# Kernel tuning notes

Hardware: AMD Instinct MI355X
Metric: run time of the kernel (lower is better)

## Reference

```python
import jax, jax.numpy as jnp
import numpy as np

ALPHA = 0.7
BETA = 0.3
GAMMA = 4.0
SMALL_LESION_WEIGHT = 10.0
SMOOTH = 1e-05
AREA_THRESH = 100  # region.area < 100 -> small lesion


def _label_components(mask):
    """8-connectivity connected-component labeling via min-label flooding.
    mask: [B,H,W] bool. Returns int32 labels in [0, H*W) for foreground,
    H*W (sentinel) for background. Equivalent partitioning to skimage.measure.label."""
    B, H, W = mask.shape
    BIG = H * W
    ids = jnp.arange(BIG, dtype=jnp.int32).reshape(1, H, W)
    lab0 = jnp.where(mask, ids, BIG)

    def neighbor_min(lab):
        p = jnp.pad(lab, ((0, 0), (1, 1), (1, 1)), constant_values=BIG)
        m = lab
        for di in range(3):  # 3x3 window = self + 8-neighbors
            for dj in range(3):
                m = jnp.minimum(m, p[:, di:di + H, dj:dj + W])
        return jnp.where(mask, m, BIG)

    def cond(state):
        return state[1]

    def body(state):
        lab, _ = state
        new = neighbor_min(lab)
        return new, jnp.any(new != lab)

    lab, _ = jax.lax.while_loop(cond, body, (lab0, jnp.array(True)))
    return lab


def _small_lesion_weights(targets):
    """targets: [B,1,H,W] float. Returns [B,1,H,W] weights: small_lesion_weight on
    pixels of connected components with area < AREA_THRESH, else 1.0."""
    t = targets[:, 0]                      # [B,H,W]
    mask = t > 0.5
    B, H, W = mask.shape
    BIG = H * W
    lab = _label_components(mask)          # [B,H,W] int32
    flat_lab = lab.reshape(B, BIG)
    ones = mask.astype(jnp.float32).reshape(B, BIG)
    # per-image component areas; background pixels fall into segment BIG
    areas = jax.vmap(lambda l, o: jax.ops.segment_sum(o, l, num_segments=BIG + 1))(flat_lab, ones)
    pix_area = jnp.take_along_axis(areas, flat_lab, axis=1).reshape(B, H, W)
    small = mask & (pix_area < AREA_THRESH)
    w = jnp.where(small, SMALL_LESION_WEIGHT, 1.0)
    return w[:, None, :, :]


def _bce_with_logits(x, t):
    # numerically stable elementwise BCE-with-logits
    return jnp.maximum(x, 0.0) - x * t + jnp.log1p(jnp.exp(-jnp.abs(x)))


def setup_inputs() -> dict:
    key = jax.random.key(0)
    k1, k2 = jax.random.split(key)
    B, C, H, W = 8, 1, 1024, 1024
    predictions = jax.random.normal(k1, (B, C, H, W), dtype=jnp.float32)
    targets = (jax.random.uniform(k2, (B, C, H, W)) < 0.05).astype(jnp.float32)
    return {"predictions": predictions, "targets": targets}


def reference(predictions, targets):
    p = jax.nn.sigmoid(predictions)

    # dice loss (global)
    inter = jnp.sum(p * targets)
    union = jnp.sum(p) + jnp.sum(targets)
    dice_loss = 1.0 - (2.0 * inter + SMOOTH) / (union + SMOOTH)

    # focal loss from logits
    bce = _bce_with_logits(predictions, targets)
    is_pos = targets == 1
    p_t = jnp.where(is_pos, p, 1.0 - p)
    alpha_t = jnp.where(is_pos, ALPHA, 1.0 - ALPHA)
    focal_loss = jnp.mean(alpha_t * (1.0 - p_t) ** GAMMA * bce)

    # tversky loss (FN-focused)
    TP = inter
    FP = jnp.sum((1.0 - targets) * p)
    FN = jnp.sum(targets * (1.0 - p))
    tversky_loss = 1.0 - (TP + SMOOTH) / (TP + ALPHA * FP + BETA * FN + SMOOTH)

    # small-lesion weighted BCE (weights are a non-diff function of targets)
    w = _small_lesion_weights(jax.lax.stop_gradient(targets))
    small_lesion_loss = jnp.mean(w * bce)

    return (dice_loss + focal_loss + tversky_loss + small_lesion_loss) / 4.0
```

## Files before the change

kernel.cpp:

```cpp
#include <hip/hip_runtime.h>

typedef unsigned int u32;
typedef unsigned long long u64;

static constexpr int Bb = 8, Hh = 1024, Ww = 1024;
static constexpr int HW     = Hh * Ww;
static constexpr int NPIX   = Bb * HW;
static constexpr int NWORDS = NPIX / 64;
static constexpr int WPR    = Ww / 64;
static constexpr int WPI    = HW / 64;
static constexpr int NBK = 2048, NT = 256;
static constexpr int FNT = 512, FBG = 512;
static constexpr int SWORDS = NWORDS / FBG;
static constexpr int SPX    = SWORDS * 64;
static constexpr int CAP    = 2048;

static constexpr u32 POISON  = 0xAAAAAAAAu;
static constexpr u32 FLAGVAL = 0xC0FFEE00u;
static constexpr u32 LBITS  = 0x3FFFu;
static constexpr u32 BIGF   = 1u << 29;
static constexpr u32 CROSSF = 1u << 30;

__device__ inline u32 lab_load(u32* L, u32 i) {
    return __hip_atomic_load(&L[i], __ATOMIC_RELAXED, __HIP_MEMORY_SCOPE_AGENT);
}
__device__ inline void lab_store(u32* L, u32 i, u32 v) {
    __hip_atomic_store(&L[i], v, __ATOMIC_RELAXED, __HIP_MEMORY_SCOPE_AGENT);
}
__device__ inline u32 find_root(u32* L, u32 x) {
    while (true) {
        u32 p = lab_load(L, x);
        if (p >= (u32)NPIX || p == x) return x;
        x = p;
    }
}
__device__ inline void union_labels(u32* L, u32 a, u32 b) {
    while (true) {
        a = find_root(L, a);
        b = find_root(L, b);
        if (a == b) return;
        if (a < b) { u32 t = a; a = b; b = t; }
        u32 old = atomicMin(&L[a], b);
        if (old == a || old >= (u32)NPIX) return;
        a = old;
    }
}

__device__ inline u32 lds_load(u32* L, u32 x) {
    return __hip_atomic_load(&L[x], __ATOMIC_RELAXED, __HIP_MEMORY_SCOPE_WORKGROUP);
}
__device__ inline void lds_store(u32* L, u32 x, u32 v) {
    __hip_atomic_store(&L[x], v, __ATOMIC_RELAXED, __HIP_MEMORY_SCOPE_WORKGROUP);
}
__device__ inline u32 lfind2(u32* L, u32 x) {
    while (true) { u32 p = lds_load(L, x) & LBITS; if (p == x) return x; x = p; }
}
__device__ inline void lunion(u32* L, u32 a, u32 b) {
    while (true) {
        a = lfind2(L, a);
        b = lfind2(L, b);
        if (a == b) return;
        if (a < b) { u32 t = a; a = b; b = t; }
        u32 old = atomicMin(&L[a], b);
        if (old == a) return;
        a = old;
    }
}

__device__ inline double block_reduce(double v, double* lds) {
    for (int o = 32; o > 0; o >>= 1) v += __shfl_down(v, o, 64);
    int wave = threadIdx.x >> 6, lane = threadIdx.x & 63;
    __syncthreads();
    if (lane == 0) lds[wave] = v;
    __syncthreads();
    double r = 0.0;
    if (threadIdx.x == 0)
        for (int w = 0; w < (int)(blockDim.x >> 6); ++w) r += lds[w];
    return r;
}

__device__ inline float bce_pos(float x) {
    return fmaxf(-x, 0.0f) + __logf(1.0f + __expf(-fabsf(x)));
}

__device__ inline u64 spread4(u64 x) {
    x &= 0xFFFFull;
    x = (x | (x << 24)) & 0x000000FF000000FFull;
    x = (x | (x << 12)) & 0x000F000F000F000Full;
    x = (x | (x << 6))  & 0x0303030303030303ull;
    x = (x | (x << 3))  & 0x1111111111111111ull;
    return x;
}

__device__ inline void grid_barrier(u32* ctr, u32* flag) {
    __syncthreads();
    if (threadIdx.x == 0) {
        u32 old = __hip_atomic_fetch_add(ctr, 1u, __ATOMIC_RELAXED,
                                         __HIP_MEMORY_SCOPE_AGENT);
        if (old == POISON + (u32)FBG - 1u) {
            __hip_atomic_store(flag, FLAGVAL, __ATOMIC_RELAXED,
                               __HIP_MEMORY_SCOPE_AGENT);
        } else {
            while (__hip_atomic_load(flag, __ATOMIC_RELAXED,
                                     __HIP_MEMORY_SCOPE_AGENT) == POISON)
                __builtin_amdgcn_s_sleep(8);
        }
    }
    __syncthreads();
}

__global__ __launch_bounds__(NT) void k_init(const float4* __restrict__ pred4,
                                             const float4* __restrict__ targ4,
                                             u64* __restrict__ mask,
                                             double* __restrict__ part) {
    __shared__ double lds[NT / 64];
    float s_p = 0.f, s_t = 0.f, s_pt = 0.f, s_f = 0.f, s_b = 0.f, s_bf = 0.f;
    const int lane = threadIdx.x & 63;
    const int wid  = (blockIdx.x * NT + threadIdx.x) >> 6;

    float4 pv[4], tv[4];
    #pragma unroll
    for (int c = 0; c < 4; ++c) {
        const int chunk = (wid << 2) + c;
        pv[c] = pred4[chunk * 64 + lane];
        tv[c] = targ4[chunk * 64 + lane];
    }
    #pragma unroll
    for (int c = 0; c < 4; ++c) {
        const int chunk = (wid << 2) + c;
        const float* xa = &pv[c].x;
        const float* ta = &tv[c].x;
        u32 nib = 0;
        #pragma unroll
        for (int b = 0; b < 4; ++b) {
            const float x = xa[b], t = ta[b];
            const float ee  = __expf(-fabsf(x));
            const float rin = __builtin_amdgcn_rcpf(1.0f + ee);
            const float p   = (x >= 0.0f) ? rin : 1.0f - rin;
            const float bce = fmaxf(x, 0.0f) - x * t + __logf(1.0f + ee);
            const bool  pos = t > 0.5f;
            const float q1  = pos ? (1.0f - p) : p;
            const float at  = pos ? 0.7f : 0.3f;
            const float q2  = q1 * q1;
            s_p  += p;
            s_t  += t;
            s_pt += pos ? p : 0.0f;
            s_f  += at * q2 * q2 * bce;
            s_b  += bce;
            s_bf += pos ? bce : 0.0f;
            if (pos) nib |= 1u << b;
        }
        const u64 B0 = __ballot(nib & 1u);
        const u64 B1 = __ballot(nib & 2u);
        const u64 B2 = __ballot(nib & 4u);
        const u64 B3 = __ballot(nib & 8u);
        const int k = lane & 3;
        const u64 W = spread4(B0 >> (16 * k)) | (spread4(B1 >> (16 * k)) << 1)
                    | (spread4(B2 >> (16 * k)) << 2) | (spread4(B3 >> (16 * k)) << 3);
        if (lane < 4) mask[(chunk << 2) + lane] = W;
    }
    double r;
    r = block_reduce((double)s_p,  lds); if (threadIdx.x == 0) part[0 * NBK + blockIdx.x] = r;
    r = block_reduce((double)s_t,  lds); if (threadIdx.x == 0) part[1 * NBK + blockIdx.x] = r;
    r = block_reduce((double)s_pt, lds); if (threadIdx.x == 0) part[2 * NBK + blockIdx.x] = r;
    r = block_reduce((double)s_f,  lds); if (threadIdx.x == 0) part[3 * NBK + blockIdx.x] = r;
    r = block_reduce((double)s_b,  lds); if (threadIdx.x == 0) part[4 * NBK + blockIdx.x] = r;
    r = block_reduce((double)s_bf, lds); if (threadIdx.x == 0) part[5 * NBK + blockIdx.x] = r;
}

struct Nbr { u64 L, R, U, UL, UR, D, DL, DR; };
__device__ inline Nbr neighbors(const u64* __restrict__ mask, int wi, u64 cur) {
    int y  = (wi & (WPI - 1)) >> 4;
    int wx = wi & (WPR - 1);
    u64 lf = wx > 0       ? mask[wi - 1] : 0;
    u64 rt = wx < WPR - 1 ? mask[wi + 1] : 0;
    u64 up = 0, ul = 0, ur = 0, dn = 0, dl = 0, dr = 0;
    if (y > 0) {
        up = mask[wi - WPR];
        ul = wx > 0       ? mask[wi - WPR - 1] : 0;
        ur = wx < WPR - 1 ? mask[wi - WPR + 1] : 0;
    }
    if (y < Hh - 1) {
        dn = mask[wi + WPR];
        dl = wx > 0       ? mask[wi + WPR - 1] : 0;
        dr = wx < WPR - 1 ? mask[wi + WPR + 1] : 0;
    }
    Nbr n;
    n.L  = (cur << 1) | (lf >> 63);
    n.R  = (cur >> 1) | (rt << 63);
    n.U  = up;
    n.UL = (up << 1) | (ul >> 63);
    n.UR = (up >> 1) | (ur << 63);
    n.D  = dn;
    n.DL = (dn << 1) | (dl >> 63);
    n.DR = (dn >> 1) | (dr << 63);
    return n;
}

__device__ inline u64 half_mask(int t) {
    return (t & 1) ? 0xFFFFFFFF00000000ull : 0x00000000FFFFFFFFull;
}

static constexpr int B_CTR1 = 0, B_FLAG1 = 32, B_CTR2 = 64, B_FLAG2 = 96, B_DONE = 128;

__global__ __launch_bounds__(FNT, 4) void k_fused(const u64* __restrict__ mask,
                                                  u32* __restrict__ lab,
                                                  u32* __restrict__ area,
                                                  const float* __restrict__ pred,
                                                  double* __restrict__ part,
                                                  u32* __restrict__ bar,
                                                  float* __restrict__ out) {
    extern __shared__ u32 llab[];
    __shared__ u32 wl[CAP];
    __shared__ u32 wl_n;
    double* part_large = part + 6 * NBK;

    const int tid   = threadIdx.x;
    const int lwi   = tid >> 1;
    const int wi    = blockIdx.x * SWORDS + lwi;
    const int spx   = blockIdx.x * SPX;
    const u64 hm    = half_mask(tid);
    const u64 cur   = mask[wi];
    const int lbase = lwi << 6;

    if (tid == 0) wl_n = 0;

    u64 nonIso = 0, nL = 0, nU = 0, nUL = 0, nUR = 0, nDany = 0;
    if (cur & hm) {
        Nbr n = neighbors(mask, wi, cur);
        nonIso = cur & (n.L | n.R | n.U | n.UL | n.UR | n.D | n.DL | n.DR) & hm;
        nL = n.L; nU = n.U; nUL = n.UL; nUR = n.UR;
        nDany = n.D | n.DL | n.DR;
    }
    __syncthreads();

    {
        int cnt = __builtin_popcountll(nonIso);
        if (cnt) {
            u32 slot = atomicAdd(&wl_n, (u32)cnt);
            u64 w = nonIso;
            while (w) {
                int b = __builtin_ctzll(w); w &= w - 1;
                const u32 li = (u32)(lbase + b);
                llab[li] = li;
                if (slot < (u32)CAP) {
                    const u32 f = (u32)((nL  >> b) & 1)
                                | ((u32)((nU  >> b) & 1) << 1)
                                | ((u32)((nUL >> b) & 1) << 2)
                                | ((u32)((nUR >> b) & 1) << 3)
                                | ((u32)((nDany >> b) & 1) << 4);
                    wl[slot] = (li << 5) | f;
                }
                ++slot;
            }
        }
    }
    __syncthreads();
    const bool fb  = wl_n > (u32)CAP;
    const u32 nwl  = fb ? 0u : wl_n;

    if (!fb) {
        for (u32 e = tid; e < nwl; e += FNT) {
            const u32 ent = wl[e], li = ent >> 5, f = ent & 31u;
            const u32 ris = li >> 10;
            if (f & 1u) lunion(llab, li, li - 1);
            if (ris > 0) {
                if (f & 2u) lunion(llab, li, li - 1024);
                else {
                    if (f & 4u) lunion(llab, li, li - 1025);
                    if (f & 8u) lunion(llab, li, li - 1023);
                }
            }
        }
        __syncthreads();
        for (u32 e = tid; e < nwl; e += FNT) {
            const u32 ent = wl[e], li = ent >> 5, f = ent & 31u;
            const u32 ris = li >> 10;
            const u32 r = lfind2(llab, li);
            if (r != li) lds_store(llab, li, r);
            atomicAdd(&llab[r], 1u << 14);
            const u32 gi = (u32)spx + li;
            if (ris == 0 && (f & (2u | 4u | 8u))) {
                atomicOr(&llab[r], CROSSF);
                const u32 gr = (u32)spx + r;
                if (f & 2u) union_labels(lab, gr, gi - Ww);
                if (f & 4u) union_labels(lab, gr, gi - Ww - 1);
                if (f & 8u) union_labels(lab, gr, gi - Ww + 1);
            }
            if (ris == 15 && (f & 16u)) {
                atomicOr(&llab[r], CROSSF);
                union_labels(lab, gi, (u32)spx + r);
            }
        }
    } else {
        u64 w = cur & (nL | nU | nUL | nUR) & hm;
        while (w) {
            int b = __builtin_ctzll(w); w &= w - 1;
            const u64 bit = 1ull << b;
            const u32 gi = (u32)(spx + lbase + b);
            if (nL & bit) union_labels(lab, gi, gi - 1);
            if (nU & bit) union_labels(lab, gi, gi - Ww);
            else {
                if (nUL & bit) union_labels(lab, gi, gi - Ww - 1);
                if (nUR & bit) union_labels(lab, gi, gi - Ww + 1);
            }
        }
    }
    grid_barrier(bar + B_CTR1, bar + B_FLAG1);

    if (!fb) {
        for (u32 e = tid; e < nwl; e += FNT) {
            const u32 li = wl[e] >> 5;
            const u32 ent = lds_load(llab, li);
            if ((ent & LBITS) != li) continue;
            if (ent & CROSSF) {
                const u32 gr = find_root(lab, (u32)spx + li);
                lab_store(lab, (u32)spx + li, gr);
                atomicAdd(&area[gr], (ent >> 14) & 0x7FFFu);
            } else if (((ent >> 14) & 0x7FFFu) >= 100u) {
                atomicOr(&llab[li], BIGF);
            }
        }
    } else {
        u64 w = nonIso;
        while (w) {
            int b = __builtin_ctzll(w); w &= w - 1;
            const u32 gi = (u32)(spx + lbase + b);
            const u32 r = find_root(lab, gi);
            lab_store(lab, gi, r);
            atomicAdd(&area[r], 1u);
        }
    }
    grid_barrier(bar + B_CTR2, bar + B_FLAG2);

    float s = 0.f;
    if (!fb) {
        for (u32 e = tid; e < nwl; e += FNT) {
            const u32 li = wl[e] >> 5;
            const u32 ent = lds_load(llab, li);
            if ((ent & LBITS) == li && (ent & CROSSF)) {
                const u32 gr  = lab_load(lab, (u32)spx + li);
                const u32 tot = __hip_atomic_load(&area[gr], __ATOMIC_RELAXED,
                                                  __HIP_MEMORY_SCOPE_AGENT) - POISON;
                if (tot >= 100u) atomicOr(&llab[li], BIGF);
            }
        }
        __syncthreads();
        for (u32 e = tid; e < nwl; e += FNT) {
            const u32 li = wl[e] >> 5;
            const u32 ent = lds_load(llab, li);
            const u32 r = ent & LBITS;
            const u32 fl = (r == li) ? ent : lds_load(llab, r);
            if (fl & BIGF) s += bce_pos(pred[spx + li]);
        }
    } else {
        u64 w = nonIso;
        while (w) {
            int b = __builtin_ctzll(w); w &= w - 1;
            const u32 gi = (u32)(spx + lbase + b);
            const u32 r = lab_load(lab, gi);
            const u32 cnt = __hip_atomic_load(&area[r], __ATOMIC_RELAXED,
                                              __HIP_MEMORY_SCOPE_AGENT) - POISON;
            if (cnt >= 100u) s += bce_pos(pred[gi]);
        }
    }
    __syncthreads();
    double* rlds   = (double*)llab;
    int* lastFlagP = (int*)&llab[32];

    double rr = block_reduce((double)s, rlds);
    if (tid == 0) {
        __hip_atomic_store(&part_large[blockIdx.x], rr, __ATOMIC_RELAXED,
                           __HIP_MEMORY_SCOPE_AGENT);
        asm volatile("s_waitcnt vmcnt(0)" ::: "memory");
        u32 old = __hip_atomic_fetch_add(bar + B_DONE, 1u, __ATOMIC_RELAXED,
                                         __HIP_MEMORY_SCOPE_AGENT);
        *lastFlagP = (old == POISON + (u32)FBG - 1u);
    }
    __syncthreads();
    if (!*lastFlagP) return;

    double sv[7] = {0, 0, 0, 0, 0, 0, 0};
    for (int j = tid; j < NBK; j += FNT)
        #pragma unroll
        for (int k = 0; k < 6; ++k) sv[k] += part[k * NBK + j];
    for (int j = tid; j < FBG; j += FNT)
        sv[6] += __hip_atomic_load(&part_large[j], __ATOMIC_RELAXED,
                                   __HIP_MEMORY_SCOPE_AGENT);
    double red[7];
    #pragma unroll
    for (int k = 0; k < 7; ++k) red[k] = block_reduce(sv[k], rlds);
    if (tid == 0) {
        double sum_p = red[0], sum_t = red[1], inter = red[2];
        double sum_f = red[3], sum_b = red[4], sum_bf = red[5], large_b = red[6];
        double small_b = sum_bf - large_b;
        double N = (double)NPIX;
        double dice    = 1.0 - (2.0 * inter + 1e-5) / (sum_p + sum_t + 1e-5);
        double focal   = sum_f / N;
        double FP = sum_p - inter, FN = sum_t - inter;
        double tversky = 1.0 - (inter + 1e-5) / (inter + 0.7 * FP + 0.3 * FN + 1e-5);
        double small   = (sum_b + 9.0 * small_b) / N;
        out[0] = (float)((dice + focal + tversky + small) * 0.25);
    }
}

extern "C" void kernel_launch(void* const* d_in, const int* in_sizes, int n_in,
                              void* d_out, int out_size, void* d_ws, size_t ws_size,
                              hipStream_t stream) {
    const float* pred = (const float*)d_in[0];
    const float* targ = (const float*)d_in[1];
    float* out = (float*)d_out;

    char* ws = (char*)d_ws;
    double* part = (double*)ws;
    u64* mask = (u64*)(ws + (size_t)(6 * NBK + FBG) * sizeof(double));
    u32* lab  = (u32*)(mask + NWORDS);
    u32* area = lab + NPIX;
    u32* bar  = area + NPIX;

    k_init <<<NBK, NT, 0, stream>>>((const float4*)pred, (const float4*)targ, mask, part);
    k_fused<<<FBG, FNT, (size_t)SPX * sizeof(u32), stream>>>(mask, lab, area, pred,
                                                             part, bar, out);
}
```

Before: 136.4 us.

## Fuse loss reduction and mask build into persistent CCL kernel with LDS mask

```diff
diff --git a/kernel.cpp b/kernel.cpp
--- a/kernel.cpp
+++ b/kernel.cpp
@@ -9,7 +9,6 @@
 static constexpr int NWORDS = NPIX / 64;
 static constexpr int WPR    = Ww / 64;
 static constexpr int WPI    = HW / 64;
-static constexpr int NBK = 2048, NT = 256;
 static constexpr int FNT = 512, FBG = 512;
 static constexpr int SWORDS = NWORDS / FBG;
 static constexpr int SPX    = SWORDS * 64;
@@ -44,6 +43,18 @@
         if (old == a || old >= (u32)NPIX) return;
         a = old;
     }
+}
+__device__ inline u64 b_load(const u64* p) {
+    return __hip_atomic_load(p, __ATOMIC_RELAXED, __HIP_MEMORY_SCOPE_AGENT);
+}
+__device__ inline void b_store(u64* p, u64 v) {
+    __hip_atomic_store(p, v, __ATOMIC_RELAXED, __HIP_MEMORY_SCOPE_AGENT);
+}
+__device__ inline double d_load(const double* p) {
+    return __hip_atomic_load(p, __ATOMIC_RELAXED, __HIP_MEMORY_SCOPE_AGENT);
+}
+__device__ inline void d_store(double* p, double v) {
+    __hip_atomic_store(p, v, __ATOMIC_RELAXED, __HIP_MEMORY_SCOPE_AGENT);
 }
 
 __device__ inline u32 lds_load(u32* L, u32 x) {
@@ -109,128 +120,139 @@
     __syncthreads();
 }
 
-__global__ __launch_bounds__(NT) void k_init(const float4* __restrict__ pred4,
-                                             const float4* __restrict__ targ4,
-                                             u64* __restrict__ mask,
-                                             double* __restrict__ part) {
-    __shared__ double lds[NT / 64];
-    float s_p = 0.f, s_t = 0.f, s_pt = 0.f, s_f = 0.f, s_b = 0.f, s_bf = 0.f;
-    const int lane = threadIdx.x & 63;
-    const int wid  = (blockIdx.x * NT + threadIdx.x) >> 6;
-
-    float4 pv[4], tv[4];
-    #pragma unroll
-    for (int c = 0; c < 4; ++c) {
-        const int chunk = (wid << 2) + c;
-        pv[c] = pred4[chunk * 64 + lane];
-        tv[c] = targ4[chunk * 64 + lane];
-    }
-    #pragma unroll
-    for (int c = 0; c < 4; ++c) {
-        const int chunk = (wid << 2) + c;
-        const float* xa = &pv[c].x;
-        const float* ta = &tv[c].x;
-        u32 nib = 0;
-        #pragma unroll
-        for (int b = 0; b < 4; ++b) {
-            const float x = xa[b], t = ta[b];
-            const float ee  = __expf(-fabsf(x));
-            const float rin = __builtin_amdgcn_rcpf(1.0f + ee);
-            const float p   = (x >= 0.0f) ? rin : 1.0f - rin;
-            const float bce = fmaxf(x, 0.0f) - x * t + __logf(1.0f + ee);
-            const bool  pos = t > 0.5f;
-            const float q1  = pos ? (1.0f - p) : p;
-            const float at  = pos ? 0.7f : 0.3f;
-            const float q2  = q1 * q1;
-            s_p  += p;
-            s_t  += t;
-            s_pt += pos ? p : 0.0f;
-            s_f  += at * q2 * q2 * bce;
-            s_b  += bce;
-            s_bf += pos ? bce : 0.0f;
-            if (pos) nib |= 1u << b;
-        }
-        const u64 B0 = __ballot(nib & 1u);
-        const u64 B1 = __ballot(nib & 2u);
-        const u64 B2 = __ballot(nib & 4u);
-        const u64 B3 = __ballot(nib & 8u);
-        const int k = lane & 3;
-        const u64 W = spread4(B0 >> (16 * k)) | (spread4(B1 >> (16 * k)) << 1)
-                    | (spread4(B2 >> (16 * k)) << 2) | (spread4(B3 >> (16 * k)) << 3);
-        if (lane < 4) mask[(chunk << 2) + lane] = W;
-    }
-    double r;
-    r = block_reduce((double)s_p,  lds); if (threadIdx.x == 0) part[0 * NBK + blockIdx.x] = r;
-    r = block_reduce((double)s_t,  lds); if (threadIdx.x == 0) part[1 * NBK + blockIdx.x] = r;
-    r = block_reduce((double)s_pt, lds); if (threadIdx.x == 0) part[2 * NBK + blockIdx.x] = r;
-    r = block_reduce((double)s_f,  lds); if (threadIdx.x == 0) part[3 * NBK + blockIdx.x] = r;
-    r = block_reduce((double)s_b,  lds); if (threadIdx.x == 0) part[4 * NBK + blockIdx.x] = r;
-    r = block_reduce((double)s_bf, lds); if (threadIdx.x == 0) part[5 * NBK + blockIdx.x] = r;
-}
-
-struct Nbr { u64 L, R, U, UL, UR, D, DL, DR; };
-__device__ inline Nbr neighbors(const u64* __restrict__ mask, int wi, u64 cur) {
-    int y  = (wi & (WPI - 1)) >> 4;
-    int wx = wi & (WPR - 1);
-    u64 lf = wx > 0       ? mask[wi - 1] : 0;
-    u64 rt = wx < WPR - 1 ? mask[wi + 1] : 0;
-    u64 up = 0, ul = 0, ur = 0, dn = 0, dl = 0, dr = 0;
-    if (y > 0) {
-        up = mask[wi - WPR];
-        ul = wx > 0       ? mask[wi - WPR - 1] : 0;
-        ur = wx < WPR - 1 ? mask[wi - WPR + 1] : 0;
-    }
-    if (y < Hh - 1) {
-        dn = mask[wi + WPR];
-        dl = wx > 0       ? mask[wi + WPR - 1] : 0;
-        dr = wx < WPR - 1 ? mask[wi + WPR + 1] : 0;
-    }
-    Nbr n;
-    n.L  = (cur << 1) | (lf >> 63);
-    n.R  = (cur >> 1) | (rt << 63);
-    n.U  = up;
-    n.UL = (up << 1) | (ul >> 63);
-    n.UR = (up >> 1) | (ur << 63);
-    n.D  = dn;
-    n.DL = (dn << 1) | (dl >> 63);
-    n.DR = (dn >> 1) | (dr << 63);
-    return n;
-}
-
 __device__ inline u64 half_mask(int t) {
     return (t & 1) ? 0xFFFFFFFF00000000ull : 0x00000000FFFFFFFFull;
 }
 
-static constexpr int B_CTR1 = 0, B_FLAG1 = 32, B_CTR2 = 64, B_FLAG2 = 96, B_DONE = 128;
-
-__global__ __launch_bounds__(FNT, 4) void k_fused(const u64* __restrict__ mask,
-                                                  u32* __restrict__ lab,
-                                                  u32* __restrict__ area,
-                                                  const float* __restrict__ pred,
-                                                  double* __restrict__ part,
-                                                  u32* __restrict__ bar,
-                                                  float* __restrict__ out) {
+static constexpr int B_CTR0 = 0,  B_FLAG0 = 32, B_CTR1 = 64, B_FLAG1 = 96;
+static constexpr int B_CTR2 = 128, B_FLAG2 = 160, B_DONE = 192;
+
+__global__ __launch_bounds__(FNT, 4) void k_all(const float4* __restrict__ pred4,
+                                                const float4* __restrict__ targ4,
+                                                u32* __restrict__ lab,
+                                                u32* __restrict__ area,
+                                                double* __restrict__ part,
+                                                u64* __restrict__ bnd,
+                                                u32* __restrict__ bar,
+                                                float* __restrict__ out) {
     extern __shared__ u32 llab[];
+    __shared__ u64 smask[SWORDS];
     __shared__ u32 wl[CAP];
     __shared__ u32 wl_n;
-    double* part_large = part + 6 * NBK;
-
-    const int tid   = threadIdx.x;
+    const float* pred = (const float*)pred4;
+    double* part_large = part + 6 * FBG;
+
+    const int b    = blockIdx.x;
+    const int tid  = threadIdx.x;
+    const int lane = tid & 63;
+    const int wv   = tid >> 6;
+    const int spx  = b * SPX;
+    double* rlds   = (double*)llab;
+
+    double d_p = 0, d_t = 0, d_pt = 0, d_f = 0, d_b = 0, d_bf = 0;
+    for (int half = 0; half < 2; ++half) {
+        float s_p = 0.f, s_t = 0.f, s_pt = 0.f, s_f = 0.f, s_b = 0.f, s_bf = 0.f;
+        float4 pv[4], tv[4];
+        #pragma unroll
+        for (int c = 0; c < 4; ++c) {
+            const int chunk = (b * 8 + wv) * 8 + half * 4 + c;
+            pv[c] = pred4[chunk * 64 + lane];
+            tv[c] = targ4[chunk * 64 + lane];
+        }
+        #pragma unroll
+        for (int c = 0; c < 4; ++c) {
+            const int chunk = (b * 8 + wv) * 8 + half * 4 + c;
+            const float* xa = &pv[c].x;
+            const float* ta = &tv[c].x;
+            u32 nib = 0;
+            #pragma unroll
+            for (int e = 0; e < 4; ++e) {
+                const float x = xa[e], t = ta[e];
+                const float ee  = __expf(-fabsf(x));
+                const float rin = __builtin_amdgcn_rcpf(1.0f + ee);
+                const float p   = (x >= 0.0f) ? rin : 1.0f - rin;
+                const float bce = fmaxf(x, 0.0f) - x * t + __logf(1.0f + ee);
+                const bool  pos = t > 0.5f;
+                const float q1  = pos ? (1.0f - p) : p;
+                const float at  = pos ? 0.7f : 0.3f;
+                const float q2  = q1 * q1;
+                s_p  += p;
+                s_t  += t;
+                s_pt += pos ? p : 0.0f;
+                s_f  += at * q2 * q2 * bce;
+                s_b  += bce;
+                s_bf += pos ? bce : 0.0f;
+                if (pos) nib |= 1u << e;
+            }
+            const u64 B0 = __ballot(nib & 1u);
+            const u64 B1 = __ballot(nib & 2u);
+            const u64 B2 = __ballot(nib & 4u);
+            const u64 B3 = __ballot(nib & 8u);
+            const int k = lane & 3;
+            const u64 W = spread4(B0 >> (16 * k)) | (spread4(B1 >> (16 * k)) << 1)
+                        | (spread4(B2 >> (16 * k)) << 2) | (spread4(B3 >> (16 * k)) << 3);
+            if (lane < 4) {
+                const int lw  = (chunk << 2) + k - b * SWORDS;
+                smask[lw] = W;
+                const int ris = lw >> 4, wx = lw & 15;
+                if (ris == 0)  b_store(&bnd[b * 32 + wx], W);
+                if (ris == 15) b_store(&bnd[b * 32 + 16 + wx], W);
+            }
+        }
+        d_p += s_p; d_t += s_t; d_pt += s_pt; d_f += s_f; d_b += s_b; d_bf += s_bf;
+    }
+    double r;
+    r = block_reduce(d_p,  rlds); if (tid == 0) d_store(&part[0 * FBG + b], r);
+    r = block_reduce(d_t,  rlds); if (tid == 0) d_store(&part[1 * FBG + b], r);
+    r = block_reduce(d_pt, rlds); if (tid == 0) d_store(&part[2 * FBG + b], r);
+    r = block_reduce(d_f,  rlds); if (tid == 0) d_store(&part[3 * FBG + b], r);
+    r = block_reduce(d_b,  rlds); if (tid == 0) d_store(&part[4 * FBG + b], r);
+    r = block_reduce(d_bf, rlds); if (tid == 0) d_store(&part[5 * FBG + b], r);
+    if (tid == 0) wl_n = 0;
+    grid_barrier(bar + B_CTR0, bar + B_FLAG0);
+
     const int lwi   = tid >> 1;
-    const int wi    = blockIdx.x * SWORDS + lwi;
-    const int spx   = blockIdx.x * SPX;
     const u64 hm    = half_mask(tid);
-    const u64 cur   = mask[wi];
+    const u64 cur   = smask[lwi];
     const int lbase = lwi << 6;
-
-    if (tid == 0) wl_n = 0;
 
     u64 nonIso = 0, nL = 0, nU = 0, nUL = 0, nUR = 0, nDany = 0;
     if (cur & hm) {
-        Nbr n = neighbors(mask, wi, cur);
-        nonIso = cur & (n.L | n.R | n.U | n.UL | n.UR | n.D | n.DL | n.DR) & hm;
-        nL = n.L; nU = n.U; nUL = n.UL; nUR = n.UR;
-        nDany = n.D | n.DL | n.DR;
+        const int ris = lwi >> 4, wx = lwi & 15;
+        const int sb  = b & 63;
+        u64 lf = wx > 0  ? smask[lwi - 1] : 0;
+        u64 rt = wx < 15 ? smask[lwi + 1] : 0;
+        u64 up = 0, ul = 0, ur = 0, dn = 0, dl = 0, dr = 0;
+        if (ris > 0) {
+            up = smask[lwi - 16];
+            ul = wx > 0  ? smask[lwi - 17] : 0;
+            ur = wx < 15 ? smask[lwi - 15] : 0;
+        } else if (sb > 0) {
+            const u64* brow = bnd + (b - 1) * 32 + 16;
+            up = b_load(brow + wx);
+            ul = wx > 0  ? b_load(brow + wx - 1) : 0;
+            ur = wx < 15 ? b_load(brow + wx + 1) : 0;
+        }
+        if (ris < 15) {
+            dn = smask[lwi + 16];
+            dl = wx > 0  ? smask[lwi + 15] : 0;
+            dr = wx < 15 ? smask[lwi + 17] : 0;
+        } else if (sb < 63) {
+            const u64* brow = bnd + (b + 1) * 32;
+            dn = b_load(brow + wx);
+            dl = wx > 0  ? b_load(brow + wx - 1) : 0;
+            dr = wx < 15 ? b_load(brow + wx + 1) : 0;
+        }
+        nL = (cur << 1) | (lf >> 63);
+        const u64 nR  = (cur >> 1) | (rt << 63);
+        nU  = up;
+        nUL = (up << 1) | (ul >> 63);
+        nUR = (up >> 1) | (ur << 63);
+        const u64 nD  = dn;
+        const u64 nDL = (dn << 1) | (dl >> 63);
+        const u64 nDR = (dn >> 1) | (dr << 63);
+        nDany = nD | nDL | nDR;
+        nonIso = cur & (nL | nR | nU | nUL | nUR | nDany) & hm;
     }
     __syncthreads();
 
@@ -240,15 +262,15 @@
             u32 slot = atomicAdd(&wl_n, (u32)cnt);
             u64 w = nonIso;
             while (w) {
-                int b = __builtin_ctzll(w); w &= w - 1;
-                const u32 li = (u32)(lbase + b);
+                int bb = __builtin_ctzll(w); w &= w - 1;
+                const u32 li = (u32)(lbase + bb);
                 llab[li] = li;
                 if (slot < (u32)CAP) {
-                    const u32 f = (u32)((nL  >> b) & 1)
-                                | ((u32)((nU  >> b) & 1) << 1)
-                                | ((u32)((nUL >> b) & 1) << 2)
-                                | ((u32)((nUR >> b) & 1) << 3)
-                                | ((u32)((nDany >> b) & 1) << 4);
+                    const u32 f = (u32)((nL  >> bb) & 1)
+                                | ((u32)((nU  >> bb) & 1) << 1)
+                                | ((u32)((nUL >> bb) & 1) << 2)
+                                | ((u32)((nUR >> bb) & 1) << 3)
+                                | ((u32)((nDany >> bb) & 1) << 4);
                     wl[slot] = (li << 5) | f;
                 }
                 ++slot;
@@ -276,28 +298,28 @@
         for (u32 e = tid; e < nwl; e += FNT) {
             const u32 ent = wl[e], li = ent >> 5, f = ent & 31u;
             const u32 ris = li >> 10;
-            const u32 r = lfind2(llab, li);
-            if (r != li) lds_store(llab, li, r);
-            atomicAdd(&llab[r], 1u << 14);
+            const u32 rr = lfind2(llab, li);
+            if (rr != li) lds_store(llab, li, rr);
+            atomicAdd(&llab[rr], 1u << 14);
             const u32 gi = (u32)spx + li;
             if (ris == 0 && (f & (2u | 4u | 8u))) {
-                atomicOr(&llab[r], CROSSF);
-                const u32 gr = (u32)spx + r;
+                atomicOr(&llab[rr], CROSSF);
+                const u32 gr = (u32)spx + rr;
                 if (f & 2u) union_labels(lab, gr, gi - Ww);
                 if (f & 4u) union_labels(lab, gr, gi - Ww - 1);
                 if (f & 8u) union_labels(lab, gr, gi - Ww + 1);
             }
             if (ris == 15 && (f & 16u)) {
-                atomicOr(&llab[r], CROSSF);
-                union_labels(lab, gi, (u32)spx + r);
+                atomicOr(&llab[rr], CROSSF);
+                union_labels(lab, gi, (u32)spx + rr);
             }
         }
     } else {
         u64 w = cur & (nL | nU | nUL | nUR) & hm;
         while (w) {
-            int b = __builtin_ctzll(w); w &= w - 1;
-            const u64 bit = 1ull << b;
-            const u32 gi = (u32)(spx + lbase + b);
+            int bb = __builtin_ctzll(w); w &= w - 1;
+            const u64 bit = 1ull << bb;
+            const u32 gi = (u32)(spx + lbase + bb);
             if (nL & bit) union_labels(lab, gi, gi - 1);
             if (nU & bit) union_labels(lab, gi, gi - Ww);
             else {
@@ -324,11 +346,11 @@
     } else {
         u64 w = nonIso;
         while (w) {
-            int b = __builtin_ctzll(w); w &= w - 1;
-            const u32 gi = (u32)(spx + lbase + b);
-            const u32 r = find_root(lab, gi);
-            lab_store(lab, gi, r);
-            atomicAdd(&area[r], 1u);
+            int bb = __builtin_ctzll(w); w &= w - 1;
+            const u32 gi = (u32)(spx + lbase + bb);
+            const u32 rr = find_root(lab, gi);
+            lab_store(lab, gi, rr);
+            atomicAdd(&area[rr], 1u);
         }
     }
     grid_barrier(bar + B_CTR2, bar + B_FLAG2);
@@ -349,29 +371,27 @@
         for (u32 e = tid; e < nwl; e += FNT) {
             const u32 li = wl[e] >> 5;
             const u32 ent = lds_load(llab, li);
-            const u32 r = ent & LBITS;
-            const u32 fl = (r == li) ? ent : lds_load(llab, r);
+            const u32 rr = ent & LBITS;
+            const u32 fl = (rr == li) ? ent : lds_load(llab, rr);
             if (fl & BIGF) s += bce_pos(pred[spx + li]);
         }
     } else {
         u64 w = nonIso;
         while (w) {
-            int b = __builtin_ctzll(w); w &= w - 1;
-            const u32 gi = (u32)(spx + lbase + b);
-            const u32 r = lab_load(lab, gi);
-            const u32 cnt = __hip_atomic_load(&area[r], __ATOMIC_RELAXED,
+            int bb = __builtin_ctzll(w); w &= w - 1;
+            const u32 gi = (u32)(spx + lbase + bb);
+            const u32 rr = lab_load(lab, gi);
+            const u32 cnt = __hip_atomic_load(&area[rr], __ATOMIC_RELAXED,
                                               __HIP_MEMORY_SCOPE_AGENT) - POISON;
             if (cnt >= 100u) s += bce_pos(pred[gi]);
         }
     }
     __syncthreads();
-    double* rlds   = (double*)llab;
     int* lastFlagP = (int*)&llab[32];
 
-    double rr = block_reduce((double)s, rlds);
+    double rr2 = block_reduce((double)s, rlds);
     if (tid == 0) {
-        __hip_atomic_store(&part_large[blockIdx.x], rr, __ATOMIC_RELAXED,
-                           __HIP_MEMORY_SCOPE_AGENT);
+        d_store(&part_large[b], rr2);
         asm volatile("s_waitcnt vmcnt(0)" ::: "memory");
         u32 old = __hip_atomic_fetch_add(bar + B_DONE, 1u, __ATOMIC_RELAXED,
                                          __HIP_MEMORY_SCOPE_AGENT);
@@ -381,12 +401,11 @@
     if (!*lastFlagP) return;
 
     double sv[7] = {0, 0, 0, 0, 0, 0, 0};
-    for (int j = tid; j < NBK; j += FNT)
+    for (int j = tid; j < FBG; j += FNT) {
         #pragma unroll
-        for (int k = 0; k < 6; ++k) sv[k] += part[k * NBK + j];
-    for (int j = tid; j < FBG; j += FNT)
-        sv[6] += __hip_atomic_load(&part_large[j], __ATOMIC_RELAXED,
-                                   __HIP_MEMORY_SCOPE_AGENT);
+        for (int k = 0; k < 6; ++k) sv[k] += d_load(&part[k * FBG + j]);
+        sv[6] += d_load(&part_large[j]);
+    }
     double red[7];
     #pragma unroll
     for (int k = 0; k < 7; ++k) red[k] = block_reduce(sv[k], rlds);
@@ -413,12 +432,11 @@
 
     char* ws = (char*)d_ws;
     double* part = (double*)ws;
-    u64* mask = (u64*)(ws + (size_t)(6 * NBK + FBG) * sizeof(double));
-    u32* lab  = (u32*)(mask + NWORDS);
+    u64* bnd  = (u64*)(ws + (size_t)(7 * FBG) * sizeof(double));
+    u32* lab  = (u32*)(bnd + (size_t)FBG * 32);
     u32* area = lab + NPIX;
     u32* bar  = area + NPIX;
 
-    k_init <<<NBK, NT, 0, stream>>>((const float4*)pred, (const float4*)targ, mask, part);
-    k_fused<<<FBG, FNT, (size_t)SPX * sizeof(u32), stream>>>(mask, lab, area, pred,
-                                                             part, bar, out);
-}
+    k_all<<<FBG, FNT, (size_t)SPX * sizeof(u32), stream>>>(
+        (const float4*)pred, (const float4*)targ, lab, area, part, bnd, bar, out);
+}
```

After: 132.7 us. 2.7% less time.
